# Performance work log

Hardware: AMD Instinct MI355X
Metric: run time of the kernel (lower is better)

## Reference

```python
import jax, jax.numpy as jnp
import numpy as np
from jax import lax

BN_EPS = 1e-5

def setup_inputs() -> dict:
    key = jax.random.key(0)
    ks = jax.random.split(key, 4)
    b, C, h, w, dim = 8, 4, 16, 16, 512
    H = 8  # num_heads
    x = jax.random.normal(ks[0], (b, C, h, w, dim), dtype=jnp.float32)
    qkv_w = jax.random.normal(ks[1], (3 * dim, dim), dtype=jnp.float32) * 0.02
    proj_w = jax.random.normal(ks[2], (dim, dim), dtype=jnp.float32) * 0.02
    proj_b = jnp.zeros((dim,), dtype=jnp.float32)
    conv_w = jax.random.normal(ks[3], (H, H, 3, 3), dtype=jnp.float32) * 0.1
    conv_b = jnp.zeros((H,), dtype=jnp.float32)
    bn_gamma = jnp.ones((H,), dtype=jnp.float32)
    bn_beta = jnp.zeros((H,), dtype=jnp.float32)
    bn_mean = jnp.zeros((H,), dtype=jnp.float32)
    bn_var = jnp.ones((H,), dtype=jnp.float32)
    return {"x": x, "qkv_w": qkv_w, "proj_w": proj_w, "proj_b": proj_b,
            "conv_w": conv_w, "conv_b": conv_b, "bn_gamma": bn_gamma,
            "bn_beta": bn_beta, "bn_mean": bn_mean, "bn_var": bn_var}


def reference(x, qkv_w, proj_w, proj_b, conv_w, conv_b, bn_gamma, bn_beta, bn_mean, bn_var):
    b, C, h, w, c = x.shape
    n = C * h * w
    H = conv_w.shape[0]            # num_heads
    hd = c // H                    # head_dim
    scale = hd ** (-0.5)

    x2 = x.reshape(b, n, c)
    qkv = x2 @ qkv_w.T             # [b, n, 3c]
    qkv = qkv.reshape(b, n, 3, H, hd)
    q = qkv[:, :, 0].transpose(0, 2, 1, 3)  # [b, H, n, hd]
    k = qkv[:, :, 1].transpose(0, 2, 1, 3)
    v = qkv[:, :, 2].transpose(0, 2, 1, 3)

    attn = jnp.einsum('bhnd,bhmd->bhnm', q * scale, k)  # [b, H, n, n]

    # dwc2: Conv2d(H->H, 3x3, pad=1) + BatchNorm2d (eval) + Sigmoid on the score matrix
    attn = lax.conv_general_dilated(attn, conv_w, (1, 1), 'SAME',
                                    dimension_numbers=('NCHW', 'OIHW', 'NCHW'))
    attn = attn + conv_b[None, :, None, None]
    inv = bn_gamma * lax.rsqrt(bn_var + BN_EPS)
    attn = attn * inv[None, :, None, None] + (bn_beta - bn_mean * inv)[None, :, None, None]
    attn = jax.nn.sigmoid(attn)

    attn = jax.nn.softmax(attn, axis=-1)
    z = jnp.einsum('bhnm,bhmd->bhnd', attn, v)           # [b, H, n, hd]
    z = z.transpose(0, 2, 1, 3).reshape(b, n, c)
    z = z @ proj_w.T + proj_b
    out = z.reshape(b, C, h, w, c) + x
    return out
```

## Files before the change

kernel.cpp:

```cpp
#include <hip/hip_runtime.h>


#define DINL __device__ __forceinline__
typedef unsigned short u16;
typedef unsigned int u32;
typedef unsigned long long u64;
typedef short bf16x8 __attribute__((ext_vector_type(8)));
typedef float f32x4 __attribute__((ext_vector_type(4)));

DINL u16 f2bf(float f) {
  u32 u = __float_as_uint(f);
  u += 0x7fffu + ((u >> 16) & 1u);
  return (u16)(u >> 16);
}
DINL float bflo(u32 u) { return __uint_as_float(u << 16); }
DINL float bfhi(u32 u) { return __uint_as_float(u & 0xffff0000u); }
DINL u32 cvtpk_bf16(float lo, float hi) {
  u32 r;
  asm("v_cvt_pk_bf16_f32 %0, %1, %2" : "=v"(r) : "v"(lo), "v"(hi));
  return r;
}
DINL u32 pk4_fp8(float a, float b, float c, float d) {
  u32 r = 0;
  r = (u32)__builtin_amdgcn_cvt_pk_fp8_f32(a, b, (int)r, false);
  r = (u32)__builtin_amdgcn_cvt_pk_fp8_f32(c, d, (int)r, true);
  return r;
}
DINL unsigned char f2fp8(float v) {
  return (unsigned char)((u32)__builtin_amdgcn_cvt_pk_fp8_f32(v, v, 0, false) & 0xffu);
}

__global__ __launch_bounds__(256) void k_cvt(const float* __restrict__ in,
                                             u16* __restrict__ out, int n8) {
  int gid = blockIdx.x * 256 + threadIdx.x;
  int stride = gridDim.x * 256;
  for (int i = gid; i < n8; i += stride) {
    float4 a = *(const float4*)&in[(size_t)i * 8];
    float4 b = *(const float4*)&in[(size_t)i * 8 + 4];
    uint4 p;
    p.x = cvtpk_bf16(a.x, a.y); p.y = cvtpk_bf16(a.z, a.w);
    p.z = cvtpk_bf16(b.x, b.y); p.w = cvtpk_bf16(b.z, b.w);
    *(uint4*)&out[(size_t)i * 8] = p;
  }
}

__global__ __launch_bounds__(256) void k_qkv(const u16* __restrict__ xb,
                                             const u16* __restrict__ wb,
                                             u16* __restrict__ Q,
                                             u16* __restrict__ K,
                                             u16* __restrict__ V) {
  __shared__ __align__(16) u16 sA[128 * 64];
  __shared__ __align__(16) u16 sB[128 * 64];
  const int tid = threadIdx.x;
  const int m0 = blockIdx.x * 128, n0 = blockIdx.y * 128;
  const int lane = tid & 63, wid = tid >> 6;
  const int wr = wid >> 1, wc = wid & 1;
  const int l15 = lane & 15, l4 = lane >> 4;
  const int row = tid >> 1, half = tid & 1, xr = row & 7;
  f32x4 acc[4][4] = {};
  for (int k0 = 0; k0 < 512; k0 += 64) {
    __syncthreads();
    {
      const u16* ga = &xb[(size_t)(m0 + row) * 512 + k0 + half * 32];
      const u16* gb = &wb[(size_t)(n0 + row) * 512 + k0 + half * 32];
#pragma unroll
      for (int q = 0; q < 4; ++q) {
        int gp = (half * 4 + q) ^ xr;
        *(uint4*)&sA[row * 64 + gp * 8] = *(const uint4*)&ga[q * 8];
        *(uint4*)&sB[row * 64 + gp * 8] = *(const uint4*)&gb[q * 8];
      }
    }
    __syncthreads();
#pragma unroll
    for (int ks = 0; ks < 2; ++ks) {
      bf16x8 af[4], bfr[4];
#pragma unroll
      for (int mr = 0; mr < 4; ++mr) {
        int rr = wr * 64 + mr * 16 + l15;
        af[mr] = *(bf16x8*)&sA[rr * 64 + ((ks * 4 + l4) ^ (rr & 7)) * 8];
      }
#pragma unroll
      for (int nr = 0; nr < 4; ++nr) {
        int rr = wc * 64 + nr * 16 + l15;
        bfr[nr] = *(bf16x8*)&sB[rr * 64 + ((ks * 4 + l4) ^ (rr & 7)) * 8];
      }
#pragma unroll
      for (int mr = 0; mr < 4; ++mr)
#pragma unroll
        for (int nr = 0; nr < 4; ++nr)
          acc[mr][nr] = __builtin_amdgcn_mfma_f32_16x16x32_bf16(af[mr], bfr[nr],
                                                                acc[mr][nr], 0, 0, 0);
    }
  }
#pragma unroll
  for (int nr = 0; nr < 4; ++nr) {
    int nn = n0 + wc * 64 + nr * 16 + l15;
    int which = nn >> 9, co = nn & 511;
    int head = co >> 6, d = co & 63;
    u16* dst = (which == 0) ? Q : (which == 1) ? K : V;
    float sc = (which == 0) ? 0.125f : 1.f;
#pragma unroll
    for (int mr = 0; mr < 4; ++mr) {
      int mb = m0 + wr * 64 + mr * 16 + l4 * 4;
#pragma unroll
      for (int r = 0; r < 4; ++r) {
        int m = mb + r;
        int bb = m >> 10, ii = m & 1023;
        dst[((((size_t)bb * 8 + head) << 10) + ii) * 64 + d] =
            f2bf(acc[mr][nr][r] * sc);
      }
    }
  }
}

__global__ __launch_bounds__(256) void k_qk(const u16* __restrict__ Q,
                                            const u16* __restrict__ Kp,
                                            unsigned char* __restrict__ S8) {
  const int bh = blockIdx.z;
  const u16* Qb = Q + (size_t)bh * 65536;
  const u16* Kb = Kp + (size_t)bh * 65536;
  __shared__ __align__(16) u16 sQ[128 * 64];
  __shared__ __align__(16) u16 sK[128 * 64];
  const int tid = threadIdx.x;
  const int m0 = blockIdx.x * 128, n0 = blockIdx.y * 128;
  {
    int row = tid >> 1, half = tid & 1;
    const u16* gq = &Qb[(size_t)(m0 + row) * 64 + half * 32];
    const u16* gk = &Kb[(size_t)(n0 + row) * 64 + half * 32];
    int xr = row & 7;
#pragma unroll
    for (int q = 0; q < 4; ++q) {
      int gp = (half * 4 + q) ^ xr;
      *(uint4*)&sQ[row * 64 + gp * 8] = *(const uint4*)&gq[q * 8];
      *(uint4*)&sK[row * 64 + gp * 8] = *(const uint4*)&gk[q * 8];
    }
  }
  __syncthreads();
  const int lane = tid & 63, wid = tid >> 6;
  const int wr = wid >> 1, wc = wid & 1;
  const int l15 = lane & 15, l4 = lane >> 4;
  f32x4 acc[4][4] = {};
  bf16x8 af[4][2], bf[4][2];
#pragma unroll
  for (int mr = 0; mr < 4; ++mr) {
    int row = wr * 64 + mr * 16 + l15;
#pragma unroll
    for (int ks = 0; ks < 2; ++ks)
      af[mr][ks] = *(bf16x8*)&sQ[row * 64 + ((ks * 4 + l4) ^ (row & 7)) * 8];
  }
#pragma unroll
  for (int nr = 0; nr < 4; ++nr) {
    int row = wc * 64 + nr * 16 + l15;
#pragma unroll
    for (int ks = 0; ks < 2; ++ks)
      bf[nr][ks] = *(bf16x8*)&sK[row * 64 + ((ks * 4 + l4) ^ (row & 7)) * 8];
  }
#pragma unroll
  for (int mr = 0; mr < 4; ++mr)
#pragma unroll
    for (int nr = 0; nr < 4; ++nr)
#pragma unroll
      for (int ks = 0; ks < 2; ++ks)
        acc[mr][nr] = __builtin_amdgcn_mfma_f32_16x16x32_bf16(af[mr][ks], bf[nr][ks],
                                                              acc[mr][nr], 0, 0, 0);
  __syncthreads();
  unsigned char* t8 = (unsigned char*)sQ;
#pragma unroll
  for (int mr = 0; mr < 4; ++mr) {
    int mloc = wr * 64 + mr * 16 + l4 * 4;
#pragma unroll
    for (int nr = 0; nr < 4; ++nr) {
      int nloc = wc * 64 + nr * 16 + l15;
#pragma unroll
      for (int r = 0; r < 4; ++r)
        t8[(mloc + r) * 128 + nloc] = f2fp8(acc[mr][nr][r]);
    }
  }
  __syncthreads();
  {
    int row = tid >> 1, c0 = (tid & 1) * 64;
    unsigned char* dst = &S8[((size_t)bh << 20) + (size_t)(m0 + row) * 1024 + n0 + c0];
#pragma unroll
    for (int q = 0; q < 4; ++q)
      *(uint4*)&dst[q * 16] = *(uint4*)&t8[row * 128 + c0 + q * 16];
  }
}

__global__ __launch_bounds__(256) void k_conv(
    const unsigned char* __restrict__ S8, unsigned char* __restrict__ P8,
    float* __restrict__ Dbuf, const float* __restrict__ cw,
    const float* __restrict__ cb, const float* __restrict__ bg,
    const float* __restrict__ bb, const float* __restrict__ bm,
    const float* __restrict__ bv) {
  const int blk = blockIdx.x;
  const int b = blk >> 10;
  const int rem = blk & 1023;
  const int ip = rem >> 1, jh = rem & 1;
  const int i0 = ip * 2, j0 = jh * 512;
  __shared__ __align__(16) unsigned char sC[514 * 40];
  __shared__ __align__(8) unsigned char sA[3][16][40];
  __shared__ float sRedD[4][16];
  const int tid = threadIdx.x;
  const int lane = tid & 63, wid = tid >> 6;
  const int l15 = lane & 15, l4 = lane >> 4;

  for (int u = tid; u < 1536; u += 256) {
    int tap = u >> 9, rem2 = u & 511;
    int m = rem2 >> 5, kk = rem2 & 31;
    int p = m >> 3, oh = m & 7;
    int ih = kk >> 2, rr = kk & 3;
    int dr = rr - p;
    float v = 0.f;
    if (dr >= 0 && dr < 3) {
      float ah = bg[oh] * rsqrtf(bv[oh] + 1e-5f);
      v = cw[((oh * 8 + ih) * 3 + dr) * 3 + tap] * ah;
    }
    sA[tap][m][kk] = f2fp8(v);
  }
  if (tid < 16) {
    int side = tid & 1, ih = tid >> 1;
    int g = side ? (j0 + 512) : (j0 - 1);
    u32 v = 0;
    if (g >= 0 && g < 1024) {
      const unsigned char* Sb = S8 + (((size_t)(b * 8 + ih)) << 20);
#pragma unroll
      for (int rr = 0; rr < 4; ++rr) {
        int r = i0 - 1 + rr;
        u32 byte = (r >= 0 && r < 1024) ? (u32)Sb[(size_t)r * 1024 + g] : 0u;
        v |= byte << (8 * rr);
      }
    }
    *(u32*)&sC[(side ? 513 : 0) * 40 + ih * 4] = v;
  }
  {
    const int ihs = tid >> 5;
    const int lc = tid & 31;
    const unsigned char* p1 =
        S8 + (((size_t)(b * 8 + ihs)) << 20) + (size_t)i0 * 1024 + j0 + lc * 4;
    const bool intr = (i0 != 0) && (i0 != 1022);
#pragma unroll
    for (int it = 0; it < 4; ++it) {
      const unsigned char* pp = p1 + it * 128;
      u32 w0, w3;
      u32 w1 = *(const u32*)pp;
      u32 w2 = *(const u32*)(pp + 1024);
      if (intr) {
        w0 = *(const u32*)(pp - 1024);
        w3 = *(const u32*)(pp + 2048);
      } else {
        w0 = (i0 != 0) ? *(const u32*)(pp - 1024) : 0u;
        w3 = (i0 != 1022) ? *(const u32*)(pp + 2048) : 0u;
      }
      u32 p01l = __builtin_amdgcn_perm(w1, w0, 0x05010400u);
      u32 p23l = __builtin_amdgcn_perm(w3, w2, 0x05010400u);
      u32 p01h = __builtin_amdgcn_perm(w1, w0, 0x07030602u);
      u32 p23h = __builtin_amdgcn_perm(w3, w2, 0x07030602u);
      unsigned char* dst = &sC[(lc * 4 + it * 128 + 1) * 40 + ihs * 4];
      *(u32*)(dst + 0)   = __builtin_amdgcn_perm(p23l, p01l, 0x05040100u);
      *(u32*)(dst + 40)  = __builtin_amdgcn_perm(p23l, p01l, 0x07060302u);
      *(u32*)(dst + 80)  = __builtin_amdgcn_perm(p23h, p01h, 0x05040100u);
      *(u32*)(dst + 120) = __builtin_amdgcn_perm(p23h, p01h, 0x07060302u);
    }
  }
  __syncthreads();

  long wfr[3];
#pragma unroll
  for (int tap = 0; tap < 3; ++tap)
    wfr[tap] = *(long*)&sA[tap][l15][l4 * 8];
  const int oh = l15 & 7, p = l15 >> 3;
  const float ah = bg[oh] * rsqrtf(bv[oh] + 1e-5f);
  const float biasm = cb[oh] * ah + bb[oh] - bm[oh] * ah;
  const int jw = wid * 128;
  unsigned char* Pst = &P8[((size_t)(b * 8 + oh) << 20) + ((size_t)(i0 + p) << 10) +
                           j0 + jw + l4 * 4];
  const unsigned char* sCb = &sC[(size_t)(jw + l15) * 40 + l4 * 8];
  float dsum = 0.f;

  for (int t = 0; t < 8; ++t) {
    f32x4 acc = {0.f, 0.f, 0.f, 0.f};
#pragma unroll
    for (int tap = 0; tap < 3; ++tap) {
      long sfr = *(long*)(sCb + t * 640 + tap * 40);
      acc = __builtin_amdgcn_mfma_f32_16x16x32_fp8_fp8(sfr, wfr[tap], acc, 0, 0, 0);
    }
    float e[4];
#pragma unroll
    for (int r = 0; r < 4; ++r) {
      float tt = acc[r] + biasm;
      float sg = 1.f / (1.f + __expf(-tt));
      e[r] = __expf(sg);
    }
    *(u32*)(Pst + t * 16) = pk4_fp8(e[0], e[1], e[2], e[3]);
    dsum += (e[0] + e[1]) + (e[2] + e[3]);
  }
  dsum += __shfl_xor(dsum, 16);
  dsum += __shfl_xor(dsum, 32);
  if (l4 == 0) sRedD[wid][l15] = dsum;
  __syncthreads();
  if (tid < 16) {
    int pp = tid >> 3, ohh = tid & 7;
    Dbuf[(size_t)jh * 65536 + ((size_t)(b * 8 + ohh) << 10) + i0 + pp] =
        sRedD[0][tid] + sRedD[1][tid] + sRedD[2][tid] + sRedD[3][tid];
  }
}

__global__ __launch_bounds__(256) void k_av(const unsigned char* __restrict__ P8,
                                            const u16* __restrict__ V,
                                            const float* __restrict__ Dbuf,
                                            u16* __restrict__ Z) {
  const int bh = blockIdx.y, m0 = blockIdx.x * 128;
  const int b = bh >> 3, h = bh & 7;
  __shared__ __align__(16) unsigned char sA8[128 * 64];
  __shared__ __align__(16) unsigned char sVt[64 * 64];
  const int tid = threadIdx.x, lane = tid & 63, wid = tid >> 6;
  const int wr = wid >> 1, wc = wid & 1, l15 = lane & 15, l4 = lane >> 4;
  f32x4 acc[4][2] = {};
  for (int k0 = 0; k0 < 1024; k0 += 64) {
    __syncthreads();
    {
      int row = tid >> 1, c0 = (tid & 1) * 32;
      const unsigned char* src =
          &P8[((size_t)bh << 20) + (size_t)(m0 + row) * 1024 + k0 + c0];
      uint4 a0 = *(const uint4*)src, a1 = *(const uint4*)(src + 16);
      u64 ul[4];
      ul[0] = (u64)a0.x | ((u64)a0.y << 32);
      ul[1] = (u64)a0.z | ((u64)a0.w << 32);
      ul[2] = (u64)a1.x | ((u64)a1.y << 32);
      ul[3] = (u64)a1.z | ((u64)a1.w << 32);
      int xr = row & 7, gb = c0 >> 3;
#pragma unroll
      for (int t = 0; t < 4; ++t)
        *(u64*)&sA8[row * 64 + ((gb + t) ^ xr) * 8] = ul[t];
    }
    {
      int j = tid >> 2, d0 = (tid & 3) * 16;
      const u16* src = &V[((size_t)bh << 16) + (size_t)(k0 + j) * 64 + d0];
      uint4 v0 = *(const uint4*)src, v1 = *(const uint4*)(src + 16);
      u32 wv[8] = {v0.x, v0.y, v0.z, v0.w, v1.x, v1.y, v1.z, v1.w};
#pragma unroll
      for (int t = 0; t < 8; ++t) {
        u32 p = (u32)__builtin_amdgcn_cvt_pk_fp8_f32(bflo(wv[t]), bfhi(wv[t]), 0, false);
        int da = d0 + t * 2, db = da + 1;
        sVt[da * 64 + (((j >> 3) ^ (da & 7)) << 3) + (j & 7)] = (unsigned char)(p & 0xff);
        sVt[db * 64 + (((j >> 3) ^ (db & 7)) << 3) + (j & 7)] = (unsigned char)((p >> 8) & 0xff);
      }
    }
    __syncthreads();
    long bfr[2][2];
#pragma unroll
    for (int nr = 0; nr < 2; ++nr) {
      int row = wc * 32 + nr * 16 + l15;
#pragma unroll
      for (int ks = 0; ks < 2; ++ks)
        bfr[nr][ks] = *(long*)&sVt[row * 64 + (((ks * 4 + l4) ^ (row & 7)) << 3)];
    }
#pragma unroll
    for (int mr = 0; mr < 4; ++mr) {
      int row = wr * 64 + mr * 16 + l15;
      long afr[2];
#pragma unroll
      for (int ks = 0; ks < 2; ++ks)
        afr[ks] = *(long*)&sA8[row * 64 + (((ks * 4 + l4) ^ (row & 7)) << 3)];
#pragma unroll
      for (int nr = 0; nr < 2; ++nr)
#pragma unroll
        for (int ks = 0; ks < 2; ++ks)
          acc[mr][nr] = __builtin_amdgcn_mfma_f32_16x16x32_fp8_fp8(afr[ks], bfr[nr][ks],
                                                                   acc[mr][nr], 0, 0, 0);
    }
  }
#pragma unroll
  for (int mr = 0; mr < 4; ++mr) {
    int mbase = m0 + wr * 64 + mr * 16 + l4 * 4;
    float dv[4];
#pragma unroll
    for (int r = 0; r < 4; ++r) {
      size_t di = ((size_t)bh << 10) + mbase + r;
      dv[r] = 1.f / (Dbuf[di] + Dbuf[di + 65536]);
    }
#pragma unroll
    for (int nr = 0; nr < 2; ++nr) {
      int d = wc * 32 + nr * 16 + l15;
#pragma unroll
      for (int r = 0; r < 4; ++r)
        Z[((size_t)(b * 1024 + mbase + r)) * 512 + h * 64 + d] =
            f2bf(acc[mr][nr][r] * dv[r]);
    }
  }
}

__global__ __launch_bounds__(256) void k_proj(const u16* __restrict__ Z,
                                              const u16* __restrict__ wb,
                                              const float* __restrict__ bias,
                                              const float* __restrict__ xin,
                                              float* __restrict__ out) {
  __shared__ __align__(16) u16 sA[128 * 64];
  __shared__ __align__(16) u16 sB[128 * 64];
  const int tid = threadIdx.x;
  const int m0 = blockIdx.x * 128, n0 = blockIdx.y * 128;
  const int lane = tid & 63, wid = tid >> 6;
  const int wr = wid >> 1, wc = wid & 1;
  const int l15 = lane & 15, l4 = lane >> 4;
  const int row = tid >> 1, half = tid & 1, xr = row & 7;
  f32x4 acc[4][4] = {};
  for (int k0 = 0; k0 < 512; k0 += 64) {
    __syncthreads();
    {
      const u16* gz = &Z[(size_t)(m0 + row) * 512 + k0 + half * 32];
      const u16* gb = &wb[(size_t)(n0 + row) * 512 + k0 + half * 32];
#pragma unroll
      for (int q = 0; q < 4; ++q) {
        int gp = (half * 4 + q) ^ xr;
        *(uint4*)&sA[row * 64 + gp * 8] = *(const uint4*)&gz[q * 8];
        *(uint4*)&sB[row * 64 + gp * 8] = *(const uint4*)&gb[q * 8];
      }
    }
    __syncthreads();
#pragma unroll
    for (int ks = 0; ks < 2; ++ks) {
      bf16x8 af[4], bfr[4];
#pragma unroll
      for (int mr = 0; mr < 4; ++mr) {
        int rr = wr * 64 + mr * 16 + l15;
        af[mr] = *(bf16x8*)&sA[rr * 64 + ((ks * 4 + l4) ^ (rr & 7)) * 8];
      }
#pragma unroll
      for (int nr = 0; nr < 4; ++nr) {
        int rr = wc * 64 + nr * 16 + l15;
        bfr[nr] = *(bf16x8*)&sB[rr * 64 + ((ks * 4 + l4) ^ (rr & 7)) * 8];
      }
#pragma unroll
      for (int mr = 0; mr < 4; ++mr)
#pragma unroll
        for (int nr = 0; nr < 4; ++nr)
          acc[mr][nr] = __builtin_amdgcn_mfma_f32_16x16x32_bf16(af[mr], bfr[nr],
                                                                acc[mr][nr], 0, 0, 0);
    }
  }
#pragma unroll
  for (int nr = 0; nr < 4; ++nr) {
    int nn = n0 + wc * 64 + nr * 16 + l15;
    float bv2 = bias[nn];
#pragma unroll
    for (int mr = 0; mr < 4; ++mr) {
      int mb = m0 + wr * 64 + mr * 16 + l4 * 4;
#pragma unroll
      for (int r = 0; r < 4; ++r) {
        size_t o = (size_t)(mb + r) * 512 + nn;
        out[o] = acc[mr][nr][r] + bv2 + xin[o];
      }
    }
  }
}

extern "C" void kernel_launch(void* const* d_in, const int* in_sizes, int n_in,
                              void* d_out, int out_size, void* d_ws, size_t ws_size,
                              hipStream_t stream) {
  const size_t need = 160ull << 20;
  if (ws_size < need) return;

  const float* x      = (const float*)d_in[0];
  const float* qkv_w  = (const float*)d_in[1];
  const float* proj_w = (const float*)d_in[2];
  const float* proj_b = (const float*)d_in[3];
  const float* conv_w = (const float*)d_in[4];
  const float* conv_b = (const float*)d_in[5];
  const float* bn_g   = (const float*)d_in[6];
  const float* bn_b   = (const float*)d_in[7];
  const float* bn_m   = (const float*)d_in[8];
  const float* bn_v   = (const float*)d_in[9];
  float* out = (float*)d_out;

  char* W = (char*)d_ws;
  u16* Wq = (u16*)W;
  float* Dbuf = (float*)W;
  u16* PWb = (u16*)(W + (1ull << 20));
  u16* Wk = (u16*)(W + (8ull << 20));
  u16* Wv = (u16*)(W + (16ull << 20));
  u16* Wz = (u16*)(W + (24ull << 20));
  unsigned char* S8 = (unsigned char*)(W + (32ull << 20));
  u16* Xb = (u16*)S8;
  u16* QWb = (u16*)(W + (40ull << 20));
  unsigned char* P8 = (unsigned char*)(W + (96ull << 20));

  k_cvt<<<2048, 256, 0, stream>>>(x, Xb, 524288);
  k_cvt<<<384, 256, 0, stream>>>(qkv_w, QWb, 98304);
  k_qkv<<<dim3(64, 12), 256, 0, stream>>>(Xb, QWb, Wq, Wk, Wv);
  k_qk<<<dim3(8, 8, 64), 256, 0, stream>>>(Wq, Wk, S8);
  k_cvt<<<128, 256, 0, stream>>>(proj_w, PWb, 32768);
  k_conv<<<dim3(8192), 256, 0, stream>>>(S8, P8, Dbuf, conv_w, conv_b, bn_g, bn_b,
                                         bn_m, bn_v);
  k_av<<<dim3(8, 64), 256, 0, stream>>>(P8, Wv, Dbuf, Wz);
  k_proj<<<dim3(64, 4), 256, 0, stream>>>(Wz, PWb, proj_b, x, out);
}
```

Baseline: 184.9 us.

## Merge input conversions and precompute folded conv/BN weights in a prep kernel

The x and qkv_w bf16 conversions are merged into one launch. The conv weight baking (folding BN scale, fp8 quantization, Toeplitz layout) and the bias fold move out of each of the 8192 k_conv blocks into a single prep kernel, which also converts proj_w. Each k_conv block then copies the prebaked 1920 bytes into shared memory with a vector load. This removes one launch and the per-block scalar weight recomputation, in exchange for an extra small global read per block.

```diff
diff --git a/kernel.cpp b/kernel.cpp
--- a/kernel.cpp
+++ b/kernel.cpp
@@ -30,17 +30,60 @@
   return (unsigned char)((u32)__builtin_amdgcn_cvt_pk_fp8_f32(v, v, 0, false) & 0xffu);
 }
 
-__global__ __launch_bounds__(256) void k_cvt(const float* __restrict__ in,
-                                             u16* __restrict__ out, int n8) {
+__global__ __launch_bounds__(256) void k_cvt_xw(const float* __restrict__ x,
+                                                const float* __restrict__ qw,
+                                                u16* __restrict__ Xb,
+                                                u16* __restrict__ QWb) {
   int gid = blockIdx.x * 256 + threadIdx.x;
   int stride = gridDim.x * 256;
-  for (int i = gid; i < n8; i += stride) {
-    float4 a = *(const float4*)&in[(size_t)i * 8];
-    float4 b = *(const float4*)&in[(size_t)i * 8 + 4];
+  for (int i = gid; i < 622592; i += stride) {
+    const float* src;
+    u16* dst;
+    size_t off;
+    if (i < 524288) { src = x; dst = Xb; off = (size_t)i * 8; }
+    else { src = qw; dst = QWb; off = (size_t)(i - 524288) * 8; }
+    float4 a = *(const float4*)&src[off];
+    float4 b = *(const float4*)&src[off + 4];
     uint4 p;
     p.x = cvtpk_bf16(a.x, a.y); p.y = cvtpk_bf16(a.z, a.w);
     p.z = cvtpk_bf16(b.x, b.y); p.w = cvtpk_bf16(b.z, b.w);
-    *(uint4*)&out[(size_t)i * 8] = p;
+    *(uint4*)&dst[off] = p;
+  }
+}
+
+__global__ __launch_bounds__(256) void k_prep(
+    const float* __restrict__ cw, const float* __restrict__ cb,
+    const float* __restrict__ bg, const float* __restrict__ bb,
+    const float* __restrict__ bm, const float* __restrict__ bv,
+    const float* __restrict__ proj_w, unsigned char* __restrict__ wbake,
+    float* __restrict__ bbake, u16* __restrict__ PWb) {
+  const int blk = blockIdx.x, tid = threadIdx.x;
+  if (blk == 0) {
+    for (int u = tid; u < 1536; u += 256) {
+      int tap = u >> 9, rem2 = u & 511;
+      int m = rem2 >> 5, kk = rem2 & 31;
+      int p = m >> 3, oh = m & 7;
+      int ih = kk >> 2, rr = kk & 3;
+      int dr = rr - p;
+      float v = 0.f;
+      if (dr >= 0 && dr < 3) {
+        float ah = bg[oh] * rsqrtf(bv[oh] + 1e-5f);
+        v = cw[((oh * 8 + ih) * 3 + dr) * 3 + tap] * ah;
+      }
+      wbake[tap * 640 + m * 40 + kk] = f2fp8(v);
+    }
+    if (tid < 8) {
+      float ah = bg[tid] * rsqrtf(bv[tid] + 1e-5f);
+      bbake[tid] = cb[tid] * ah + bb[tid] - bm[tid] * ah;
+    }
+  } else {
+    int i = (blk - 1) * 256 + tid;
+    float4 a = *(const float4*)&proj_w[(size_t)i * 8];
+    float4 b = *(const float4*)&proj_w[(size_t)i * 8 + 4];
+    uint4 p;
+    p.x = cvtpk_bf16(a.x, a.y); p.y = cvtpk_bf16(a.z, a.w);
+    p.z = cvtpk_bf16(b.x, b.y); p.w = cvtpk_bf16(b.z, b.w);
+    *(uint4*)&PWb[(size_t)i * 8] = p;
   }
 }
 
@@ -188,37 +231,24 @@
 
 __global__ __launch_bounds__(256) void k_conv(
     const unsigned char* __restrict__ S8, unsigned char* __restrict__ P8,
-    float* __restrict__ Dbuf, const float* __restrict__ cw,
-    const float* __restrict__ cb, const float* __restrict__ bg,
-    const float* __restrict__ bb, const float* __restrict__ bm,
-    const float* __restrict__ bv) {
+    float* __restrict__ Dbuf, const unsigned char* __restrict__ wbake,
+    const float* __restrict__ bbake) {
   const int blk = blockIdx.x;
   const int b = blk >> 10;
   const int rem = blk & 1023;
   const int ip = rem >> 1, jh = rem & 1;
   const int i0 = ip * 2, j0 = jh * 512;
   __shared__ __align__(16) unsigned char sC[514 * 40];
-  __shared__ __align__(8) unsigned char sA[3][16][40];
+  __shared__ __align__(16) unsigned char sA[3][16][40];
   __shared__ float sRedD[4][16];
   const int tid = threadIdx.x;
   const int lane = tid & 63, wid = tid >> 6;
   const int l15 = lane & 15, l4 = lane >> 4;
 
-  for (int u = tid; u < 1536; u += 256) {
-    int tap = u >> 9, rem2 = u & 511;
-    int m = rem2 >> 5, kk = rem2 & 31;
-    int p = m >> 3, oh = m & 7;
-    int ih = kk >> 2, rr = kk & 3;
-    int dr = rr - p;
-    float v = 0.f;
-    if (dr >= 0 && dr < 3) {
-      float ah = bg[oh] * rsqrtf(bv[oh] + 1e-5f);
-      v = cw[((oh * 8 + ih) * 3 + dr) * 3 + tap] * ah;
-    }
-    sA[tap][m][kk] = f2fp8(v);
-  }
-  if (tid < 16) {
-    int side = tid & 1, ih = tid >> 1;
+  if (tid < 120) ((uint4*)sA)[tid] = ((const uint4*)wbake)[tid];
+  if (tid >= 120 && tid < 136) {
+    int t = tid - 120;
+    int side = t & 1, ih = t >> 1;
     int g = side ? (j0 + 512) : (j0 - 1);
     u32 v = 0;
     if (g >= 0 && g < 1024) {
@@ -269,8 +299,7 @@
   for (int tap = 0; tap < 3; ++tap)
     wfr[tap] = *(long*)&sA[tap][l15][l4 * 8];
   const int oh = l15 & 7, p = l15 >> 3;
-  const float ah = bg[oh] * rsqrtf(bv[oh] + 1e-5f);
-  const float biasm = cb[oh] * ah + bb[oh] - bm[oh] * ah;
+  const float biasm = bbake[oh];
   const int jw = wid * 128;
   unsigned char* Pst = &P8[((size_t)(b * 8 + oh) << 20) + ((size_t)(i0 + p) << 10) +
                            j0 + jw + l4 * 4];
@@ -476,6 +505,8 @@
   u16* Wq = (u16*)W;
   float* Dbuf = (float*)W;
   u16* PWb = (u16*)(W + (1ull << 20));
+  unsigned char* wbake = (unsigned char*)(W + (2ull << 20));
+  float* bbake = (float*)(W + (2ull << 20) + 4096);
   u16* Wk = (u16*)(W + (8ull << 20));
   u16* Wv = (u16*)(W + (16ull << 20));
   u16* Wz = (u16*)(W + (24ull << 20));
@@ -484,13 +515,12 @@
   u16* QWb = (u16*)(W + (40ull << 20));
   unsigned char* P8 = (unsigned char*)(W + (96ull << 20));
 
-  k_cvt<<<2048, 256, 0, stream>>>(x, Xb, 524288);
-  k_cvt<<<384, 256, 0, stream>>>(qkv_w, QWb, 98304);
+  k_cvt_xw<<<2048, 256, 0, stream>>>(x, qkv_w, Xb, QWb);
   k_qkv<<<dim3(64, 12), 256, 0, stream>>>(Xb, QWb, Wq, Wk, Wv);
   k_qk<<<dim3(8, 8, 64), 256, 0, stream>>>(Wq, Wk, S8);
-  k_cvt<<<128, 256, 0, stream>>>(proj_w, PWb, 32768);
-  k_conv<<<dim3(8192), 256, 0, stream>>>(S8, P8, Dbuf, conv_w, conv_b, bn_g, bn_b,
-                                         bn_m, bn_v);
+  k_prep<<<129, 256, 0, stream>>>(conv_w, conv_b, bn_g, bn_b, bn_m, bn_v,
+                                  proj_w, wbake, bbake, PWb);
+  k_conv<<<dim3(8192), 256, 0, stream>>>(S8, P8, Dbuf, wbake, bbake);
   k_av<<<dim3(8, 64), 256, 0, stream>>>(P8, Wv, Dbuf, Wz);
   k_proj<<<dim3(64, 4), 256, 0, stream>>>(Wz, PWb, proj_b, x, out);
 }
```

Result: faster. 162.1 us (-12.3%).
